# Kernel tuning notes

Measured on AMD Instinct MI355X. Metric: run time of the kernel, lower is better.

Reference implementation:

```python
import jax, jax.numpy as jnp
import numpy as np

N_NODES = 100000
N_GRAPHS = 256
HIDDEN = 64
IN_DIM = 512


def gcn_conv(x, edge_index, W, b, n_nodes):
    """PyG GCNConv: out = D^{-1/2} (A+I) D^{-1/2} (x W) + b."""
    h = x @ W  # [N, H] -- transform first (as PyG does), messages are small
    src = jnp.concatenate([edge_index[0], jnp.arange(n_nodes)])  # add self loops
    dst = jnp.concatenate([edge_index[1], jnp.arange(n_nodes)])
    ones = jnp.ones(src.shape[0], dtype=h.dtype)
    deg = jax.ops.segment_sum(ones, dst, num_segments=n_nodes)
    dinv = jnp.where(deg > 0, jax.lax.rsqrt(deg), 0.0)
    norm = dinv[src] * dinv[dst]  # [E+N]
    msg = h[src] * norm[:, None]  # gather + scale
    out = jax.ops.segment_sum(msg, dst, num_segments=n_nodes)  # scatter-add
    return out + b


def global_mean_pool(x, batch, num_graphs):
    s = jax.ops.segment_sum(x, batch, num_segments=num_graphs)
    cnt = jax.ops.segment_sum(jnp.ones(x.shape[0], dtype=x.dtype), batch,
                              num_segments=num_graphs)
    return s / jnp.maximum(cnt, 1.0)[:, None]


def setup_inputs() -> dict:
    key = jax.random.key(0)
    ks = jax.random.split(key, 9)
    x = jax.random.normal(ks[0], (N_NODES, IN_DIM), dtype=jnp.float32)
    edge_index = jax.random.randint(ks[1], (2, 1600000), 0, N_NODES, dtype=jnp.int64) \
        if jax.config.jax_enable_x64 else jax.random.randint(ks[1], (2, 1600000), 0, N_NODES).astype(jnp.int32)
    batch = jnp.sort(jax.random.randint(ks[2], (N_NODES,), 0, N_GRAPHS))
    sc1 = 1.0 / np.sqrt(IN_DIM)
    sc2 = 1.0 / np.sqrt(HIDDEN)
    W1 = jax.random.uniform(ks[3], (IN_DIM, HIDDEN), minval=-sc1, maxval=sc1, dtype=jnp.float32)
    b1 = jnp.zeros((HIDDEN,), dtype=jnp.float32)
    W2 = jax.random.uniform(ks[4], (HIDDEN, HIDDEN), minval=-sc2, maxval=sc2, dtype=jnp.float32)
    b2 = jnp.zeros((HIDDEN,), dtype=jnp.float32)
    Wfc = jax.random.uniform(ks[5], (HIDDEN, 1), minval=-sc2, maxval=sc2, dtype=jnp.float32)
    bfc = jnp.zeros((1,), dtype=jnp.float32)
    return {"x": x, "edge_index": edge_index, "batch": batch,
            "W1": W1, "b1": b1, "W2": W2, "b2": b2, "Wfc": Wfc, "bfc": bfc}


def reference(x, edge_index, batch, W1, b1, W2, b2, Wfc, bfc):
    n = x.shape[0]
    h = jax.nn.relu(gcn_conv(x, edge_index, W1, b1, n))
    h = jax.nn.relu(gcn_conv(h, edge_index, W2, b2, n))
    g = global_mean_pool(h, batch, N_GRAPHS)  # [G, H]
    out = g @ Wfc + bfc  # [G, 1]
    return out.squeeze(-1)
```

## Files before the change

kernel.cpp:

```cpp
#include <hip/hip_runtime.h>

#define HIDDEN 64
#define IN_DIM 512
#define CAP 4096
#define NB_MAX 1024

typedef short v8s __attribute__((ext_vector_type(8)));
typedef float v4f __attribute__((ext_vector_type(4)));

static __device__ __forceinline__ unsigned short f2bf(float f) {
    unsigned int u = __float_as_uint(f);
    u = (u + 0x7FFF + ((u >> 16) & 1)) >> 16;
    return (unsigned short)u;
}
static __device__ __forceinline__ float bf2f(unsigned short u) {
    return __uint_as_float(((unsigned int)u) << 16);
}
static __device__ __forceinline__ float bflo(unsigned u) { return __uint_as_float(u << 16); }
static __device__ __forceinline__ float bfhi(unsigned u) { return __uint_as_float(u & 0xffff0000u); }

__global__ void k_init(int* cursor, float* gsum, int* gcnt) {
    int i = blockIdx.x * 256 + threadIdx.x;
    if (i < NB_MAX) cursor[i] = 0;
    if (i < 256) { gsum[i] = 0.f; gcnt[i] = 0; }
}

__launch_bounds__(256)
__global__ void k_bin(const int* __restrict__ src, const int* __restrict__ dst,
                      int* cursor, unsigned* __restrict__ bucket_data, int n_edges) {
    __shared__ unsigned words[4096];
    __shared__ unsigned short binsh[4096];
    __shared__ int hist[NB_MAX];
    __shared__ int base[NB_MAX];
    const int tid = threadIdx.x;
    const int e0 = blockIdx.x * 4096;
    for (int i = tid; i < NB_MAX; i += 256) hist[i] = 0;
    __syncthreads();
    for (int i = tid; i < 4096; i += 256) {
        int e = e0 + i;
        if (e < n_edges) {
            int d = dst[e], s = src[e];
            words[i] = ((unsigned)s << 7) | (unsigned)(d & 127);
            int b = d >> 7;
            binsh[i] = (unsigned short)b;
            atomicAdd(&hist[b], 1);
        } else binsh[i] = 0xFFFFu;
    }
    __syncthreads();
    for (int b = tid; b < NB_MAX; b += 256) {
        int c = hist[b];
        base[b] = c ? atomicAdd(&cursor[b], c) : 0;
        hist[b] = 0;
    }
    __syncthreads();
    for (int i = tid; i < 4096; i += 256) {
        unsigned short b = binsh[i];
        if (b != 0xFFFFu) {
            int slot = atomicAdd(&hist[b], 1);
            int p = base[b] + slot;
            if (p < CAP) bucket_data[(size_t)b * CAP + p] = words[i];
        }
    }
}

__launch_bounds__(256)
__global__ void k_bexc(const int* __restrict__ cursor, int* __restrict__ bucket_base,
                       int* __restrict__ row_start, int n_nodes, int nbuck) {
    __shared__ int wsum[4];
    const int t = threadIdx.x, lane = t & 63, w = t >> 6;
    int v[4], s = 0;
#pragma unroll
    for (int k = 0; k < 4; ++k) {
        int i = t * 4 + k;
        int c = (i < nbuck) ? cursor[i] : 0;
        if (c > CAP) c = CAP;
        v[k] = s; s += c;
    }
    int inc = s;
#pragma unroll
    for (int off = 1; off < 64; off <<= 1) {
        int u = __shfl_up(inc, off, 64);
        if (lane >= off) inc += u;
    }
    if (lane == 63) wsum[w] = inc;
    __syncthreads();
    int cross = 0;
    for (int i = 0; i < w; ++i) cross += wsum[i];
    int b0 = cross + inc - s;
#pragma unroll
    for (int k = 0; k < 4; ++k) {
        int i = t * 4 + k;
        if (i < NB_MAX) bucket_base[i] = b0 + v[k];
    }
    if (t == 255) row_start[n_nodes] = cross + inc;
}

__launch_bounds__(256)
__global__ void k_csr(const unsigned* __restrict__ bucket_data, const int* __restrict__ cursor,
                      const int* __restrict__ bucket_base,
                      int* __restrict__ row_start, int* __restrict__ csr,
                      float* __restrict__ dinv, int n_nodes) {
    __shared__ unsigned words[CAP];
    __shared__ int cnt[128];
    __shared__ int loff[128];
    __shared__ int cur[128];
    __shared__ int w0sum;
    const int tid = threadIdx.x, bin = blockIdx.x, n0 = bin << 7;
    int c = cursor[bin]; if (c > CAP) c = CAP;
    const unsigned* bd = bucket_data + (size_t)bin * CAP;
    for (int i = tid; i < c; i += 256) words[i] = bd[i];
    if (tid < 128) { cnt[tid] = 0; cur[tid] = 0; }
    __syncthreads();
    for (int i = tid; i < c; i += 256) atomicAdd(&cnt[words[i] & 127], 1);
    __syncthreads();
    int val = 0, inc = 0;
    if (tid < 128) {
        const int lane = tid & 63;
        val = cnt[tid];
        inc = val;
#pragma unroll
        for (int off = 1; off < 64; off <<= 1) {
            int u = __shfl_up(inc, off, 64);
            if (lane >= off) inc += u;
        }
        if (tid == 63) w0sum = inc;
    }
    __syncthreads();
    if (tid < 128) {
        int excl = inc - val + ((tid >= 64) ? w0sum : 0);
        loff[tid] = excl;
        int n = n0 + tid;
        if (n < n_nodes) {
            row_start[n] = bucket_base[bin] + excl;
            dinv[n] = rsqrtf((float)(val + 1));
        }
    }
    __syncthreads();
    const int gbase = bucket_base[bin];
    for (int i = tid; i < c; i += 256) {
        unsigned wd = words[i];
        int d = wd & 127;
        int slot = atomicAdd(&cur[d], 1);
        csr[gbase + loff[d] + slot] = (int)(wd >> 7);
    }
}

__global__ void k_prep(const float* __restrict__ W1, unsigned short* __restrict__ Wt) {
    int idx = blockIdx.x * 256 + threadIdx.x;
    int n = idx >> 9, k = idx & 511;
    Wt[(size_t)n * 512 + k] = f2bf(W1[(size_t)k * 64 + n]);
}

__launch_bounds__(256)
__global__ void k_gemm1m(const float* __restrict__ x, const unsigned short* __restrict__ Wt,
                         const float* __restrict__ dinv, unsigned short* __restrict__ s1,
                         int n_nodes) {
    __shared__ __align__(16) unsigned short lX[64 * 136];
    __shared__ __align__(16) unsigned short lW[64 * 136];
    const int tid  = threadIdx.x;
    const int lane = tid & 63;
    const int w    = tid >> 6;
    const int quad = lane >> 4;
    const int m16  = lane & 15;
    const int row0 = blockIdx.x * 64;

    v4f acc[4];
#pragma unroll
    for (int b = 0; b < 4; ++b) acc[b] = (v4f){0.f, 0.f, 0.f, 0.f};

    for (int kc = 0; kc < IN_DIM; kc += 128) {
        __syncthreads();
#pragma unroll
        for (int i = 0; i < 8; ++i) {
            int fidx = tid + i * 256;
            int r  = fidx >> 5;
            int c4 = fidx & 31;
            int gr = row0 + r;
            float4 v = make_float4(0.f, 0.f, 0.f, 0.f);
            if (gr < n_nodes) v = ((const float4*)(x + (size_t)gr * IN_DIM + kc))[c4];
            ushort4 u = make_ushort4(f2bf(v.x), f2bf(v.y), f2bf(v.z), f2bf(v.w));
            *(ushort4*)(lX + r * 136 + c4 * 4) = u;
        }
#pragma unroll
        for (int i = 0; i < 4; ++i) {
            int idx = tid + i * 256;
            int n  = idx >> 4;
            int c8 = idx & 15;
            uint4 u = *(const uint4*)(Wt + (size_t)n * 512 + kc + c8 * 8);
            *(uint4*)(lW + n * 136 + c8 * 8) = u;
        }
        __syncthreads();
#pragma unroll
        for (int kk = 0; kk < 128; kk += 32) {
            v8s a = *(const v8s*)(lX + (w * 16 + m16) * 136 + kk + quad * 8);
#pragma unroll
            for (int b = 0; b < 4; ++b) {
                v8s bb = *(const v8s*)(lW + (b * 16 + m16) * 136 + kk + quad * 8);
                acc[b] = __builtin_amdgcn_mfma_f32_16x16x32_bf16(a, bb, acc[b], 0, 0, 0);
            }
        }
    }
    __syncthreads();
    float* lC = (float*)lX;
#pragma unroll
    for (int b = 0; b < 4; ++b)
#pragma unroll
        for (int r = 0; r < 4; ++r) {
            int rowt = w * 16 + quad * 4 + r;
            lC[rowt * 65 + b * 16 + m16] = acc[b][r];
        }
    __syncthreads();
#pragma unroll
    for (int i = 0; i < 2; ++i) {
        int base = i * 2048 + tid * 8;
        int r = base >> 6;
        int c = base & 63;
        int gr = row0 + r;
        if (gr < n_nodes) {
            float d = dinv[gr];
            const float* p = lC + r * 65 + c;
            unsigned p0 = (unsigned)f2bf(p[0] * d) | ((unsigned)f2bf(p[1] * d) << 16);
            unsigned p1 = (unsigned)f2bf(p[2] * d) | ((unsigned)f2bf(p[3] * d) << 16);
            unsigned p2 = (unsigned)f2bf(p[4] * d) | ((unsigned)f2bf(p[5] * d) << 16);
            unsigned p3 = (unsigned)f2bf(p[6] * d) | ((unsigned)f2bf(p[7] * d) << 16);
            *(uint4*)(s1 + (size_t)gr * 64 + c) = make_uint4(p0, p1, p2, p3);
        }
    }
}

#define NPW 4

__launch_bounds__(256)
__global__ void k_layer1(const unsigned short* __restrict__ sin, const int* __restrict__ row_start,
                         const int* __restrict__ csr, const float* __restrict__ W2,
                         const float* __restrict__ b1, const float* __restrict__ dinv,
                         unsigned short* __restrict__ sout, int n_nodes) {
    __shared__ float ldsW[HIDDEN * HIDDEN];
    const int tid = threadIdx.x;
    {
        const float4* Wg = (const float4*)W2;
        float4* Wl = (float4*)ldsW;
#pragma unroll
        for (int i = 0; i < 4; ++i) Wl[tid + i * 256] = Wg[tid + i * 256];
    }
    __syncthreads();
    const int lane = tid & 63;
    const int wave = tid >> 6;
    const int g = lane >> 4;
    const int l = lane & 15;
    const float4 b4 = ((const float4*)b1)[l];
    const int n0 = (blockIdx.x * 4 + wave) * NPW;
    if (n0 >= n_nodes) return;

    int rs_nxt = row_start[n0];
    int idx_nxt = csr[rs_nxt + lane];
    uint2 us_nxt = *(const uint2*)(sin + (size_t)n0 * HIDDEN + l * 4);

    for (int i = 0; i < NPW; ++i) {
        int n = n0 + i;
        if (n >= n_nodes) break;
        const int rs = rs_nxt;
        const int re = row_start[n + 1];
        const int idx = idx_nxt;
        const uint2 uself = us_nxt;
        if (i + 1 < NPW && n + 1 < n_nodes) {
            rs_nxt = re;
            idx_nxt = csr[re + lane];
            us_nxt = *(const uint2*)(sin + (size_t)(n + 1) * HIDDEN + l * 4);
        }

        float4 acc = make_float4(0.f, 0.f, 0.f, 0.f);
        int m0 = re - rs; if (m0 > 64) m0 = 64;
        int mq = (m0 + 3) >> 2;
#pragma unroll 4
        for (int jq = 0; jq < mq; ++jq) {
            int myj = jq * 4 + g;
            int cm = myj < m0 ? myj : 0;
            int a = __shfl(idx, cm, 64);
            uint2 u = *(const uint2*)(sin + (size_t)a * HIDDEN + l * 4);
            if (myj < m0) {
                acc.x += bflo(u.x); acc.y += bfhi(u.x);
                acc.z += bflo(u.y); acc.w += bfhi(u.y);
            }
        }
        if (__builtin_expect(re - rs > 64, 0)) {
            for (int base = rs + 64; base < re; base += 64) {
                int idx2 = csr[base + lane];
                int m = re - base; if (m > 64) m = 64;
                int mq2 = (m + 3) >> 2;
#pragma unroll 4
                for (int jq = 0; jq < mq2; ++jq) {
                    int myj = jq * 4 + g;
                    int cm = myj < m ? myj : 0;
                    int a = __shfl(idx2, cm, 64);
                    uint2 u = *(const uint2*)(sin + (size_t)a * HIDDEN + l * 4);
                    if (myj < m) {
                        acc.x += bflo(u.x); acc.y += bfhi(u.x);
                        acc.z += bflo(u.y); acc.w += bfhi(u.y);
                    }
                }
            }
        }
        acc.x += __shfl_xor(acc.x, 16, 64); acc.y += __shfl_xor(acc.y, 16, 64);
        acc.z += __shfl_xor(acc.z, 16, 64); acc.w += __shfl_xor(acc.w, 16, 64);
        acc.x += __shfl_xor(acc.x, 32, 64); acc.y += __shfl_xor(acc.y, 32, 64);
        acc.z += __shfl_xor(acc.z, 32, 64); acc.w += __shfl_xor(acc.w, 32, 64);
        acc.x += bflo(uself.x); acc.y += bfhi(uself.x);
        acc.z += bflo(uself.y); acc.w += bfhi(uself.y);
        float d = dinv[n];
        float4 h;
        h.x = fmaxf(fmaf(d, acc.x, b4.x), 0.f);
        h.y = fmaxf(fmaf(d, acc.y, b4.y), 0.f);
        h.z = fmaxf(fmaf(d, acc.z, b4.z), 0.f);
        h.w = fmaxf(fmaf(d, acc.w, b4.w), 0.f);
        float4 a4 = make_float4(0.f, 0.f, 0.f, 0.f);
#pragma unroll
        for (int kk = 0; kk < 16; ++kk) {
            int srcl = 4 * g + (kk >> 2);
            float hk;
            if ((kk & 3) == 0)      hk = __shfl(h.x, srcl, 64);
            else if ((kk & 3) == 1) hk = __shfl(h.y, srcl, 64);
            else if ((kk & 3) == 2) hk = __shfl(h.z, srcl, 64);
            else                    hk = __shfl(h.w, srcl, 64);
            float4 w4 = *(const float4*)(ldsW + (16 * g + kk) * HIDDEN + 4 * l);
            a4.x = fmaf(hk, w4.x, a4.x);
            a4.y = fmaf(hk, w4.y, a4.y);
            a4.z = fmaf(hk, w4.z, a4.z);
            a4.w = fmaf(hk, w4.w, a4.w);
        }
        a4.x += __shfl_xor(a4.x, 16, 64); a4.y += __shfl_xor(a4.y, 16, 64);
        a4.z += __shfl_xor(a4.z, 16, 64); a4.w += __shfl_xor(a4.w, 16, 64);
        a4.x += __shfl_xor(a4.x, 32, 64); a4.y += __shfl_xor(a4.y, 32, 64);
        a4.z += __shfl_xor(a4.z, 32, 64); a4.w += __shfl_xor(a4.w, 32, 64);
        if (g == 0) {
            unsigned p0 = (unsigned)f2bf(a4.x * d) | ((unsigned)f2bf(a4.y * d) << 16);
            unsigned p1 = (unsigned)f2bf(a4.z * d) | ((unsigned)f2bf(a4.w * d) << 16);
            *(uint2*)(sout + (size_t)n * HIDDEN + l * 4) = make_uint2(p0, p1);
        }
    }
}

__launch_bounds__(256)
__global__ void k_layer2pool(const unsigned short* __restrict__ sin, const int* __restrict__ row_start,
                             const int* __restrict__ csr, const float* __restrict__ b2,
                             const float* __restrict__ dinv, const float* __restrict__ Wfc,
                             const int* __restrict__ batch,
                             float* gsum, int* gcnt, int n_nodes) {
    __shared__ float lsum[256];
    __shared__ int   lcnt[256];
    const int tid = threadIdx.x;
    lsum[tid] = 0.f; lcnt[tid] = 0;
    __syncthreads();
    const int lane = tid & 63;
    const int wave = tid >> 6;
    const int g = lane >> 4;
    const int l = lane & 15;
    const float4 b4  = ((const float4*)b2)[l];
    const float4 wf4 = ((const float4*)Wfc)[l];
    const int n0 = (blockIdx.x * 4 + wave) * NPW;
    if (n0 < n_nodes) {
        int rs_nxt = row_start[n0];
        int idx_nxt = csr[rs_nxt + lane];
        uint2 us_nxt = *(const uint2*)(sin + (size_t)n0 * HIDDEN + l * 4);

        for (int i = 0; i < NPW; ++i) {
            int n = n0 + i;
            if (n >= n_nodes) break;
            const int rs = rs_nxt;
            const int re = row_start[n + 1];
            const int idx = idx_nxt;
            const uint2 uself = us_nxt;
            if (i + 1 < NPW && n + 1 < n_nodes) {
                rs_nxt = re;
                idx_nxt = csr[re + lane];
                us_nxt = *(const uint2*)(sin + (size_t)(n + 1) * HIDDEN + l * 4);
            }

            float4 acc = make_float4(0.f, 0.f, 0.f, 0.f);
            int m0 = re - rs; if (m0 > 64) m0 = 64;
            int mq = (m0 + 3) >> 2;
#pragma unroll 4
            for (int jq = 0; jq < mq; ++jq) {
                int myj = jq * 4 + g;
                int cm = myj < m0 ? myj : 0;
                int a = __shfl(idx, cm, 64);
                uint2 u = *(const uint2*)(sin + (size_t)a * HIDDEN + l * 4);
                if (myj < m0) {
                    acc.x += bflo(u.x); acc.y += bfhi(u.x);
                    acc.z += bflo(u.y); acc.w += bfhi(u.y);
                }
            }
            if (__builtin_expect(re - rs > 64, 0)) {
                for (int base = rs + 64; base < re; base += 64) {
                    int idx2 = csr[base + lane];
                    int m = re - base; if (m > 64) m = 64;
                    int mq2 = (m + 3) >> 2;
#pragma unroll 4
                    for (int jq = 0; jq < mq2; ++jq) {
                        int myj = jq * 4 + g;
                        int cm = myj < m ? myj : 0;
                        int a = __shfl(idx2, cm, 64);
                        uint2 u = *(const uint2*)(sin + (size_t)a * HIDDEN + l * 4);
                        if (myj < m) {
                            acc.x += bflo(u.x); acc.y += bfhi(u.x);
                            acc.z += bflo(u.y); acc.w += bfhi(u.y);
                        }
                    }
                }
            }
            acc.x += __shfl_xor(acc.x, 16, 64); acc.y += __shfl_xor(acc.y, 16, 64);
            acc.z += __shfl_xor(acc.z, 16, 64); acc.w += __shfl_xor(acc.w, 16, 64);
            acc.x += __shfl_xor(acc.x, 32, 64); acc.y += __shfl_xor(acc.y, 32, 64);
            acc.z += __shfl_xor(acc.z, 32, 64); acc.w += __shfl_xor(acc.w, 32, 64);
            acc.x += bflo(uself.x); acc.y += bfhi(uself.x);
            acc.z += bflo(uself.y); acc.w += bfhi(uself.y);
            float d = dinv[n];
            float t = fmaxf(fmaf(d, acc.x, b4.x), 0.f) * wf4.x
                    + fmaxf(fmaf(d, acc.y, b4.y), 0.f) * wf4.y
                    + fmaxf(fmaf(d, acc.z, b4.z), 0.f) * wf4.z
                    + fmaxf(fmaf(d, acc.w, b4.w), 0.f) * wf4.w;
#pragma unroll
            for (int off = 8; off; off >>= 1) t += __shfl_down(t, off, 16);
            if (lane == 0) {
                int gr = batch[n];
                atomicAdd(&lsum[gr], t);
                atomicAdd(&lcnt[gr], 1);
            }
        }
    }
    __syncthreads();
    if (lcnt[tid]) {
        atomicAdd(&gsum[tid], lsum[tid]);
        atomicAdd(&gcnt[tid], lcnt[tid]);
    }
}

__global__ void k_out(const float* __restrict__ gsum, const int* __restrict__ gcnt,
                      const float* __restrict__ bfc, float* out) {
    int g = threadIdx.x;
    if (g < 256) {
        float c = (float)(gcnt[g] > 1 ? gcnt[g] : 1);
        out[g] = gsum[g] / c + bfc[0];
    }
}

extern "C" void kernel_launch(void* const* d_in, const int* in_sizes, int n_in,
                              void* d_out, int out_size, void* d_ws, size_t ws_size,
                              hipStream_t stream) {
    const float* x   = (const float*)d_in[0];
    const int*   ei  = (const int*)d_in[1];
    const int*   bat = (const int*)d_in[2];
    const float* W1  = (const float*)d_in[3];
    const float* b1  = (const float*)d_in[4];
    const float* W2  = (const float*)d_in[5];
    const float* b2  = (const float*)d_in[6];
    const float* Wfc = (const float*)d_in[7];
    const float* bfc = (const float*)d_in[8];
    float* out = (float*)d_out;

    const int n_nodes = in_sizes[2];
    const int n_edges = in_sizes[1] / 2;
    const int* src = ei;
    const int* dst = ei + n_edges;
    const int NBUCK = (n_nodes + 127) >> 7;

    char* w = (char*)d_ws;
    size_t off = 0;
    auto alloc = [&](size_t bytes) -> void* {
        void* p = w + off;
        off += (bytes + 255) & ~(size_t)255;
        return p;
    };
    float* dinv = (float*)alloc((size_t)n_nodes * sizeof(float));
    unsigned short* bufA = (unsigned short*)alloc((size_t)n_nodes * HIDDEN * 2);
    unsigned short* bufB = (unsigned short*)alloc((size_t)n_nodes * HIDDEN * 2);
    unsigned short* Wt   = (unsigned short*)alloc((size_t)HIDDEN * IN_DIM * 2);
    float* gsum = (float*)alloc(256 * sizeof(float));
    int*   gcnt = (int*)  alloc(256 * sizeof(int));
    int*   cursor      = (int*)alloc((size_t)NB_MAX * sizeof(int));
    int*   bucket_base = (int*)alloc((size_t)NB_MAX * sizeof(int));
    unsigned* bucket_data = (unsigned*)alloc((size_t)NB_MAX * CAP * sizeof(unsigned));
    int* row_start = (int*)alloc(((size_t)n_nodes + 1) * sizeof(int));
    int* csr       = (int*)alloc(((size_t)n_edges + 64) * sizeof(int));
    (void)ws_size; (void)n_in; (void)out_size;

    hipLaunchKernelGGL(k_init, dim3(NB_MAX / 256), dim3(256), 0, stream, cursor, gsum, gcnt);
    hipLaunchKernelGGL(k_bin, dim3((n_edges + 4095) / 4096), dim3(256), 0, stream,
                       src, dst, cursor, bucket_data, n_edges);
    hipLaunchKernelGGL(k_bexc, dim3(1), dim3(256), 0, stream,
                       cursor, bucket_base, row_start, n_nodes, NBUCK);
    hipLaunchKernelGGL(k_csr, dim3(NBUCK), dim3(256), 0, stream,
                       bucket_data, cursor, bucket_base, row_start, csr, dinv, n_nodes);
    hipLaunchKernelGGL(k_prep, dim3((HIDDEN * IN_DIM) / 256), dim3(256), 0, stream, W1, Wt);
    hipLaunchKernelGGL(k_gemm1m, dim3((n_nodes + 63) / 64), dim3(256), 0, stream,
                       x, Wt, dinv, bufA, n_nodes);
    const int gb = (n_nodes + 4 * NPW - 1) / (4 * NPW);
    hipLaunchKernelGGL(k_layer1, dim3(gb), dim3(256), 0, stream,
                       bufA, row_start, csr, W2, b1, dinv, bufB, n_nodes);
    hipLaunchKernelGGL(k_layer2pool, dim3(gb), dim3(256), 0, stream,
                       bufB, row_start, csr, b2, dinv, Wfc, bat, gsum, gcnt, n_nodes);
    hipLaunchKernelGGL(k_out, dim3(1), dim3(256), 0, stream, gsum, gcnt, bfc, out);
}
```

Measured before the change: 492.5 us.

## Use zero sentinel row and byte offsets in gather, keep W2 in registers

Adds a zero padding row at index n_nodes in both feature buffers, initialized in k_init, so out-of-range gather lanes read zeros instead of being masked. The CSR now stores byte offsets (src*128) rather than node indices, which removes the multiply from address computation. The layer-1 kernel holds its slice of W2 in registers instead of staging it in LDS with a block barrier. These changes cut branches, address arithmetic and LDS traffic in the gather loop, at the cost of extra loads for padded lanes and higher register pressure.

```diff
diff --git a/kernel.cpp b/kernel.cpp
--- a/kernel.cpp
+++ b/kernel.cpp
@@ -19,10 +19,15 @@
 static __device__ __forceinline__ float bflo(unsigned u) { return __uint_as_float(u << 16); }
 static __device__ __forceinline__ float bfhi(unsigned u) { return __uint_as_float(u & 0xffff0000u); }
 
-__global__ void k_init(int* cursor, float* gsum, int* gcnt) {
+__global__ void k_init(int* cursor, float* gsum, int* gcnt,
+                       unsigned short* bufA, unsigned short* bufB, int n_nodes) {
     int i = blockIdx.x * 256 + threadIdx.x;
     if (i < NB_MAX) cursor[i] = 0;
     if (i < 256) { gsum[i] = 0.f; gcnt[i] = 0; }
+    if (i < 64) {
+        bufA[(size_t)n_nodes * 64 + i] = 0;
+        bufB[(size_t)n_nodes * 64 + i] = 0;
+    }
 }
 
 __launch_bounds__(256)
@@ -141,7 +146,7 @@
         unsigned wd = words[i];
         int d = wd & 127;
         int slot = atomicAdd(&cur[d], 1);
-        csr[gbase + loff[d] + slot] = (int)(wd >> 7);
+        csr[gbase + loff[d] + slot] = (int)(wd & 0xFFFFFF80u);
     }
 }
 
@@ -235,26 +240,25 @@
                          const int* __restrict__ csr, const float* __restrict__ W2,
                          const float* __restrict__ b1, const float* __restrict__ dinv,
                          unsigned short* __restrict__ sout, int n_nodes) {
-    __shared__ float ldsW[HIDDEN * HIDDEN];
     const int tid = threadIdx.x;
-    {
-        const float4* Wg = (const float4*)W2;
-        float4* Wl = (float4*)ldsW;
-#pragma unroll
-        for (int i = 0; i < 4; ++i) Wl[tid + i * 256] = Wg[tid + i * 256];
-    }
-    __syncthreads();
     const int lane = tid & 63;
     const int wave = tid >> 6;
     const int g = lane >> 4;
     const int l = lane & 15;
     const float4 b4 = ((const float4*)b1)[l];
+    float4 wreg[16];
+#pragma unroll
+    for (int kk = 0; kk < 16; ++kk)
+        wreg[kk] = *(const float4*)(W2 + (size_t)(16 * g + kk) * HIDDEN + 4 * l);
+
     const int n0 = (blockIdx.x * 4 + wave) * NPW;
     if (n0 >= n_nodes) return;
+    const char* sp = (const char*)sin;
+    const int zoff = n_nodes * (HIDDEN * 2);
 
     int rs_nxt = row_start[n0];
     int idx_nxt = csr[rs_nxt + lane];
-    uint2 us_nxt = *(const uint2*)(sin + (size_t)n0 * HIDDEN + l * 4);
+    uint2 us_nxt = *(const uint2*)(sp + (size_t)n0 * 128 + l * 8);
 
     for (int i = 0; i < NPW; ++i) {
         int n = n0 + i;
@@ -266,7 +270,7 @@
         if (i + 1 < NPW && n + 1 < n_nodes) {
             rs_nxt = re;
             idx_nxt = csr[re + lane];
-            us_nxt = *(const uint2*)(sin + (size_t)(n + 1) * HIDDEN + l * 4);
+            us_nxt = *(const uint2*)(sp + (size_t)(n + 1) * 128 + l * 8);
         }
 
         float4 acc = make_float4(0.f, 0.f, 0.f, 0.f);
@@ -275,13 +279,11 @@
 #pragma unroll 4
         for (int jq = 0; jq < mq; ++jq) {
             int myj = jq * 4 + g;
-            int cm = myj < m0 ? myj : 0;
-            int a = __shfl(idx, cm, 64);
-            uint2 u = *(const uint2*)(sin + (size_t)a * HIDDEN + l * 4);
-            if (myj < m0) {
-                acc.x += bflo(u.x); acc.y += bfhi(u.x);
-                acc.z += bflo(u.y); acc.w += bfhi(u.y);
-            }
+            int a = __shfl(idx, myj, 64);
+            a = (myj < m0) ? a : zoff;
+            uint2 u = *(const uint2*)(sp + (size_t)(unsigned)a + l * 8);
+            acc.x += bflo(u.x); acc.y += bfhi(u.x);
+            acc.z += bflo(u.y); acc.w += bfhi(u.y);
         }
         if (__builtin_expect(re - rs > 64, 0)) {
             for (int base = rs + 64; base < re; base += 64) {
@@ -291,13 +293,11 @@
 #pragma unroll 4
                 for (int jq = 0; jq < mq2; ++jq) {
                     int myj = jq * 4 + g;
-                    int cm = myj < m ? myj : 0;
-                    int a = __shfl(idx2, cm, 64);
-                    uint2 u = *(const uint2*)(sin + (size_t)a * HIDDEN + l * 4);
-                    if (myj < m) {
-                        acc.x += bflo(u.x); acc.y += bfhi(u.x);
-                        acc.z += bflo(u.y); acc.w += bfhi(u.y);
-                    }
+                    int a = __shfl(idx2, myj, 64);
+                    a = (myj < m) ? a : zoff;
+                    uint2 u = *(const uint2*)(sp + (size_t)(unsigned)a + l * 8);
+                    acc.x += bflo(u.x); acc.y += bfhi(u.x);
+                    acc.z += bflo(u.y); acc.w += bfhi(u.y);
                 }
             }
         }
@@ -322,11 +322,10 @@
             else if ((kk & 3) == 1) hk = __shfl(h.y, srcl, 64);
             else if ((kk & 3) == 2) hk = __shfl(h.z, srcl, 64);
             else                    hk = __shfl(h.w, srcl, 64);
-            float4 w4 = *(const float4*)(ldsW + (16 * g + kk) * HIDDEN + 4 * l);
-            a4.x = fmaf(hk, w4.x, a4.x);
-            a4.y = fmaf(hk, w4.y, a4.y);
-            a4.z = fmaf(hk, w4.z, a4.z);
-            a4.w = fmaf(hk, w4.w, a4.w);
+            a4.x = fmaf(hk, wreg[kk].x, a4.x);
+            a4.y = fmaf(hk, wreg[kk].y, a4.y);
+            a4.z = fmaf(hk, wreg[kk].z, a4.z);
+            a4.w = fmaf(hk, wreg[kk].w, a4.w);
         }
         a4.x += __shfl_xor(a4.x, 16, 64); a4.y += __shfl_xor(a4.y, 16, 64);
         a4.z += __shfl_xor(a4.z, 16, 64); a4.w += __shfl_xor(a4.w, 16, 64);
@@ -359,9 +358,11 @@
     const float4 wf4 = ((const float4*)Wfc)[l];
     const int n0 = (blockIdx.x * 4 + wave) * NPW;
     if (n0 < n_nodes) {
+        const char* sp = (const char*)sin;
+        const int zoff = n_nodes * (HIDDEN * 2);
         int rs_nxt = row_start[n0];
         int idx_nxt = csr[rs_nxt + lane];
-        uint2 us_nxt = *(const uint2*)(sin + (size_t)n0 * HIDDEN + l * 4);
+        uint2 us_nxt = *(const uint2*)(sp + (size_t)n0 * 128 + l * 8);
 
         for (int i = 0; i < NPW; ++i) {
             int n = n0 + i;
@@ -373,7 +374,7 @@
             if (i + 1 < NPW && n + 1 < n_nodes) {
                 rs_nxt = re;
                 idx_nxt = csr[re + lane];
-                us_nxt = *(const uint2*)(sin + (size_t)(n + 1) * HIDDEN + l * 4);
+                us_nxt = *(const uint2*)(sp + (size_t)(n + 1) * 128 + l * 8);
             }
 
             float4 acc = make_float4(0.f, 0.f, 0.f, 0.f);
@@ -382,13 +383,11 @@
 #pragma unroll 4
             for (int jq = 0; jq < mq; ++jq) {
                 int myj = jq * 4 + g;
-                int cm = myj < m0 ? myj : 0;
-                int a = __shfl(idx, cm, 64);
-                uint2 u = *(const uint2*)(sin + (size_t)a * HIDDEN + l * 4);
-                if (myj < m0) {
-                    acc.x += bflo(u.x); acc.y += bfhi(u.x);
-                    acc.z += bflo(u.y); acc.w += bfhi(u.y);
-                }
+                int a = __shfl(idx, myj, 64);
+                a = (myj < m0) ? a : zoff;
+                uint2 u = *(const uint2*)(sp + (size_t)(unsigned)a + l * 8);
+                acc.x += bflo(u.x); acc.y += bfhi(u.x);
+                acc.z += bflo(u.y); acc.w += bfhi(u.y);
             }
             if (__builtin_expect(re - rs > 64, 0)) {
                 for (int base = rs + 64; base < re; base += 64) {
@@ -398,13 +397,11 @@
 #pragma unroll 4
                     for (int jq = 0; jq < mq2; ++jq) {
                         int myj = jq * 4 + g;
-                        int cm = myj < m ? myj : 0;
-                        int a = __shfl(idx2, cm, 64);
-                        uint2 u = *(const uint2*)(sin + (size_t)a * HIDDEN + l * 4);
-                        if (myj < m) {
-                            acc.x += bflo(u.x); acc.y += bfhi(u.x);
-                            acc.z += bflo(u.y); acc.w += bfhi(u.y);
-                        }
+                        int a = __shfl(idx2, myj, 64);
+                        a = (myj < m) ? a : zoff;
+                        uint2 u = *(const uint2*)(sp + (size_t)(unsigned)a + l * 8);
+                        acc.x += bflo(u.x); acc.y += bfhi(u.x);
+                        acc.z += bflo(u.y); acc.w += bfhi(u.y);
                     }
                 }
             }
@@ -472,8 +469,8 @@
         return p;
     };
     float* dinv = (float*)alloc((size_t)n_nodes * sizeof(float));
-    unsigned short* bufA = (unsigned short*)alloc((size_t)n_nodes * HIDDEN * 2);
-    unsigned short* bufB = (unsigned short*)alloc((size_t)n_nodes * HIDDEN * 2);
+    unsigned short* bufA = (unsigned short*)alloc(((size_t)n_nodes + 1) * HIDDEN * 2);
+    unsigned short* bufB = (unsigned short*)alloc(((size_t)n_nodes + 1) * HIDDEN * 2);
     unsigned short* Wt   = (unsigned short*)alloc((size_t)HIDDEN * IN_DIM * 2);
     float* gsum = (float*)alloc(256 * sizeof(float));
     int*   gcnt = (int*)  alloc(256 * sizeof(int));
@@ -484,7 +481,8 @@
     int* csr       = (int*)alloc(((size_t)n_edges + 64) * sizeof(int));
     (void)ws_size; (void)n_in; (void)out_size;
 
-    hipLaunchKernelGGL(k_init, dim3(NB_MAX / 256), dim3(256), 0, stream, cursor, gsum, gcnt);
+    hipLaunchKernelGGL(k_init, dim3(NB_MAX / 256), dim3(256), 0, stream,
+                       cursor, gsum, gcnt, bufA, bufB, n_nodes);
     hipLaunchKernelGGL(k_bin, dim3((n_edges + 4095) / 4096), dim3(256), 0, stream,
                        src, dst, cursor, bucket_data, n_edges);
     hipLaunchKernelGGL(k_bexc, dim3(1), dim3(256), 0, stream,
```

New measurement: 513.8 us. 1.04x slower.

## Split layer-1 aggregation from W2 transform and run transform on MFMA

Applied to the files above, without the earlier changes.

The fused layer-1 kernel, which did the 64x64 W2 product per node with shuffles and LDS FMAs, is split into an aggregation-only kernel that writes fp32 aggregates and a separate bf16 MFMA GEMM kernel that applies bias, ReLU, W2 and dinv scaling. The aim is to take the per-node scalar matmul and shuffle overhead off the latency-bound gather kernel. In exchange it adds a 25.6 MB fp32 intermediate round-trip through memory, one more kernel launch, and bf16 rounding of the ReLU output before the GEMM.

```diff
diff --git a/kernel.cpp b/kernel.cpp
--- a/kernel.cpp
+++ b/kernel.cpp
@@ -145,10 +145,17 @@
     }
 }
 
-__global__ void k_prep(const float* __restrict__ W1, unsigned short* __restrict__ Wt) {
+__global__ void k_prep(const float* __restrict__ W1, const float* __restrict__ W2,
+                       unsigned short* __restrict__ Wt, unsigned short* __restrict__ Wt2) {
     int idx = blockIdx.x * 256 + threadIdx.x;
-    int n = idx >> 9, k = idx & 511;
-    Wt[(size_t)n * 512 + k] = f2bf(W1[(size_t)k * 64 + n]);
+    if (idx < HIDDEN * IN_DIM) {
+        int n = idx >> 9, k = idx & 511;
+        Wt[(size_t)n * 512 + k] = f2bf(W1[(size_t)k * 64 + n]);
+    } else {
+        int j = idx - HIDDEN * IN_DIM;
+        int n = j >> 6, k = j & 63;
+        Wt2[(size_t)n * 64 + k] = f2bf(W2[(size_t)k * 64 + n]);
+    }
 }
 
 __launch_bounds__(256)
@@ -231,24 +238,14 @@
 #define NPW 4
 
 __launch_bounds__(256)
-__global__ void k_layer1(const unsigned short* __restrict__ sin, const int* __restrict__ row_start,
-                         const int* __restrict__ csr, const float* __restrict__ W2,
-                         const float* __restrict__ b1, const float* __restrict__ dinv,
-                         unsigned short* __restrict__ sout, int n_nodes) {
-    __shared__ float ldsW[HIDDEN * HIDDEN];
+__global__ void k_agg1(const unsigned short* __restrict__ sin, const int* __restrict__ row_start,
+                       const int* __restrict__ csr, const float* __restrict__ dinv,
+                       float* __restrict__ tout, int n_nodes) {
     const int tid = threadIdx.x;
-    {
-        const float4* Wg = (const float4*)W2;
-        float4* Wl = (float4*)ldsW;
-#pragma unroll
-        for (int i = 0; i < 4; ++i) Wl[tid + i * 256] = Wg[tid + i * 256];
-    }
-    __syncthreads();
     const int lane = tid & 63;
     const int wave = tid >> 6;
     const int g = lane >> 4;
     const int l = lane & 15;
-    const float4 b4 = ((const float4*)b1)[l];
     const int n0 = (blockIdx.x * 4 + wave) * NPW;
     if (n0 >= n_nodes) return;
 
@@ -308,34 +305,87 @@
         acc.x += bflo(uself.x); acc.y += bfhi(uself.x);
         acc.z += bflo(uself.y); acc.w += bfhi(uself.y);
         float d = dinv[n];
-        float4 h;
-        h.x = fmaxf(fmaf(d, acc.x, b4.x), 0.f);
-        h.y = fmaxf(fmaf(d, acc.y, b4.y), 0.f);
-        h.z = fmaxf(fmaf(d, acc.z, b4.z), 0.f);
-        h.w = fmaxf(fmaf(d, acc.w, b4.w), 0.f);
-        float4 a4 = make_float4(0.f, 0.f, 0.f, 0.f);
-#pragma unroll
-        for (int kk = 0; kk < 16; ++kk) {
-            int srcl = 4 * g + (kk >> 2);
-            float hk;
-            if ((kk & 3) == 0)      hk = __shfl(h.x, srcl, 64);
-            else if ((kk & 3) == 1) hk = __shfl(h.y, srcl, 64);
-            else if ((kk & 3) == 2) hk = __shfl(h.z, srcl, 64);
-            else                    hk = __shfl(h.w, srcl, 64);
-            float4 w4 = *(const float4*)(ldsW + (16 * g + kk) * HIDDEN + 4 * l);
-            a4.x = fmaf(hk, w4.x, a4.x);
-            a4.y = fmaf(hk, w4.y, a4.y);
-            a4.z = fmaf(hk, w4.z, a4.z);
-            a4.w = fmaf(hk, w4.w, a4.w);
-        }
-        a4.x += __shfl_xor(a4.x, 16, 64); a4.y += __shfl_xor(a4.y, 16, 64);
-        a4.z += __shfl_xor(a4.z, 16, 64); a4.w += __shfl_xor(a4.w, 16, 64);
-        a4.x += __shfl_xor(a4.x, 32, 64); a4.y += __shfl_xor(a4.y, 32, 64);
-        a4.z += __shfl_xor(a4.z, 32, 64); a4.w += __shfl_xor(a4.w, 32, 64);
         if (g == 0) {
-            unsigned p0 = (unsigned)f2bf(a4.x * d) | ((unsigned)f2bf(a4.y * d) << 16);
-            unsigned p1 = (unsigned)f2bf(a4.z * d) | ((unsigned)f2bf(a4.w * d) << 16);
-            *(uint2*)(sout + (size_t)n * HIDDEN + l * 4) = make_uint2(p0, p1);
+            float4 t4 = make_float4(d * acc.x, d * acc.y, d * acc.z, d * acc.w);
+            *(float4*)(tout + (size_t)n * HIDDEN + l * 4) = t4;
+        }
+    }
+}
+
+__launch_bounds__(256)
+__global__ void k_gemm2m(const float* __restrict__ tin, const unsigned short* __restrict__ Wt2,
+                         const float* __restrict__ b1, const float* __restrict__ dinv,
+                         unsigned short* __restrict__ sout, int n_nodes) {
+    __shared__ __align__(16) unsigned short lX[64 * 136];
+    __shared__ __align__(16) unsigned short lW[64 * 72];
+    const int tid  = threadIdx.x;
+    const int lane = tid & 63;
+    const int w    = tid >> 6;
+    const int quad = lane >> 4;
+    const int m16  = lane & 15;
+    const int row0 = blockIdx.x * 64;
+
+#pragma unroll
+    for (int i = 0; i < 4; ++i) {
+        int fidx = tid + i * 256;
+        int r  = fidx >> 4;
+        int c4 = fidx & 15;
+        int gr = row0 + r;
+        float4 v = make_float4(0.f, 0.f, 0.f, 0.f);
+        if (gr < n_nodes) v = ((const float4*)(tin + (size_t)gr * HIDDEN))[c4];
+        float4 bb = ((const float4*)b1)[c4];
+        v.x = fmaxf(v.x + bb.x, 0.f);
+        v.y = fmaxf(v.y + bb.y, 0.f);
+        v.z = fmaxf(v.z + bb.z, 0.f);
+        v.w = fmaxf(v.w + bb.w, 0.f);
+        ushort4 u = make_ushort4(f2bf(v.x), f2bf(v.y), f2bf(v.z), f2bf(v.w));
+        *(ushort4*)(lX + r * 72 + c4 * 4) = u;
+    }
+#pragma unroll
+    for (int i = 0; i < 2; ++i) {
+        int idx = tid + i * 256;
+        int n  = idx >> 3;
+        int c8 = idx & 7;
+        uint4 u = *(const uint4*)(Wt2 + (size_t)n * 64 + c8 * 8);
+        *(uint4*)(lW + n * 72 + c8 * 8) = u;
+    }
+    __syncthreads();
+    v4f acc[4];
+#pragma unroll
+    for (int b = 0; b < 4; ++b) acc[b] = (v4f){0.f, 0.f, 0.f, 0.f};
+#pragma unroll
+    for (int kk = 0; kk < 64; kk += 32) {
+        v8s a = *(const v8s*)(lX + (w * 16 + m16) * 72 + kk + quad * 8);
+#pragma unroll
+        for (int b = 0; b < 4; ++b) {
+            v8s bb = *(const v8s*)(lW + (b * 16 + m16) * 72 + kk + quad * 8);
+            acc[b] = __builtin_amdgcn_mfma_f32_16x16x32_bf16(a, bb, acc[b], 0, 0, 0);
+        }
+    }
+    __syncthreads();
+    float* lC = (float*)lX;
+#pragma unroll
+    for (int b = 0; b < 4; ++b)
+#pragma unroll
+        for (int r = 0; r < 4; ++r) {
+            int rowt = w * 16 + quad * 4 + r;
+            lC[rowt * 65 + b * 16 + m16] = acc[b][r];
+        }
+    __syncthreads();
+#pragma unroll
+    for (int i = 0; i < 2; ++i) {
+        int base = i * 2048 + tid * 8;
+        int r = base >> 6;
+        int c = base & 63;
+        int gr = row0 + r;
+        if (gr < n_nodes) {
+            float d = dinv[gr];
+            const float* p = lC + r * 65 + c;
+            unsigned p0 = (unsigned)f2bf(p[0] * d) | ((unsigned)f2bf(p[1] * d) << 16);
+            unsigned p1 = (unsigned)f2bf(p[2] * d) | ((unsigned)f2bf(p[3] * d) << 16);
+            unsigned p2 = (unsigned)f2bf(p[4] * d) | ((unsigned)f2bf(p[5] * d) << 16);
+            unsigned p3 = (unsigned)f2bf(p[6] * d) | ((unsigned)f2bf(p[7] * d) << 16);
+            *(uint4*)(sout + (size_t)gr * 64 + c) = make_uint4(p0, p1, p2, p3);
         }
     }
 }
@@ -474,7 +524,9 @@
     float* dinv = (float*)alloc((size_t)n_nodes * sizeof(float));
     unsigned short* bufA = (unsigned short*)alloc((size_t)n_nodes * HIDDEN * 2);
     unsigned short* bufB = (unsigned short*)alloc((size_t)n_nodes * HIDDEN * 2);
+    float* tbuf = (float*)alloc((size_t)n_nodes * HIDDEN * sizeof(float));
     unsigned short* Wt   = (unsigned short*)alloc((size_t)HIDDEN * IN_DIM * 2);
+    unsigned short* Wt2  = (unsigned short*)alloc((size_t)HIDDEN * HIDDEN * 2);
     float* gsum = (float*)alloc(256 * sizeof(float));
     int*   gcnt = (int*)  alloc(256 * sizeof(int));
     int*   cursor      = (int*)alloc((size_t)NB_MAX * sizeof(int));
@@ -491,12 +543,15 @@
                        cursor, bucket_base, row_start, n_nodes, NBUCK);
     hipLaunchKernelGGL(k_csr, dim3(NBUCK), dim3(256), 0, stream,
                        bucket_data, cursor, bucket_base, row_start, csr, dinv, n_nodes);
-    hipLaunchKernelGGL(k_prep, dim3((HIDDEN * IN_DIM) / 256), dim3(256), 0, stream, W1, Wt);
+    hipLaunchKernelGGL(k_prep, dim3((HIDDEN * IN_DIM + HIDDEN * HIDDEN) / 256), dim3(256), 0, stream,
+                       W1, W2, Wt, Wt2);
     hipLaunchKernelGGL(k_gemm1m, dim3((n_nodes + 63) / 64), dim3(256), 0, stream,
                        x, Wt, dinv, bufA, n_nodes);
     const int gb = (n_nodes + 4 * NPW - 1) / (4 * NPW);
-    hipLaunchKernelGGL(k_layer1, dim3(gb), dim3(256), 0, stream,
-                       bufA, row_start, csr, W2, b1, dinv, bufB, n_nodes);
+    hipLaunchKernelGGL(k_agg1, dim3(gb), dim3(256), 0, stream,
+                       bufA, row_start, csr, dinv, tbuf, n_nodes);
+    hipLaunchKernelGGL(k_gemm2m, dim3((n_nodes + 63) / 64), dim3(256), 0, stream,
+                       tbuf, Wt2, b1, dinv, bufB, n_nodes);
     hipLaunchKernelGGL(k_layer2pool, dim3(gb), dim3(256), 0, stream,
                        bufB, row_start, csr, b2, dinv, Wfc, bat, gsum, gcnt, n_nodes);
     hipLaunchKernelGGL(k_out, dim3(1), dim3(256), 0, stream, gsum, gcnt, bfc, out);
```

Result: faster. 473.0 us (-4.0%).
